# Kernel tuning notes

Hardware: AMD Instinct MI355X
Metric: run time of the kernel (lower is better)

## Reference

```python
import jax, jax.numpy as jnp
import numpy as np

B, LIMG, LTXT = 1, 2048, 256
H, NH, HD = 3072, 24, 128
MLP = int(H * 4.0)
EPS = 1e-6


def setup_inputs() -> dict:
    key = jax.random.key(0)
    ks = iter(jax.random.split(key, 64))
    rn = lambda shape, s=0.02: jax.random.normal(next(ks), shape, jnp.float32) * s
    inp = {
        'img': jax.random.normal(next(ks), (B, LIMG, H), jnp.float32),
        'txt': jax.random.normal(next(ks), (B, LTXT, H), jnp.float32),
        'vec': jax.random.normal(next(ks), (B, H), jnp.float32),
        'pe': jax.random.normal(next(ks), (1, 1, LTXT + LIMG, HD // 2, 2, 2), jnp.float32),
    }
    for p in ('img', 'txt'):
        inp[f'{p}_mod_w'] = rn((H, 6 * H)); inp[f'{p}_mod_b'] = jnp.zeros((6 * H,), jnp.float32)
        inp[f'{p}_ln1_s'] = jnp.ones((H,), jnp.float32); inp[f'{p}_ln1_b'] = jnp.zeros((H,), jnp.float32)
        inp[f'{p}_qkv_w'] = rn((H, 3 * H)); inp[f'{p}_qkv_b'] = jnp.zeros((3 * H,), jnp.float32)
        inp[f'{p}_qn'] = jnp.ones((HD,), jnp.float32); inp[f'{p}_kn'] = jnp.ones((HD,), jnp.float32)
        inp[f'{p}_proj_w'] = rn((H, H)); inp[f'{p}_proj_b'] = jnp.zeros((H,), jnp.float32)
        inp[f'{p}_ln2_s'] = jnp.ones((H,), jnp.float32); inp[f'{p}_ln2_b'] = jnp.zeros((H,), jnp.float32)
        inp[f'{p}_mlp_w1'] = rn((H, MLP)); inp[f'{p}_mlp_b1'] = jnp.zeros((MLP,), jnp.float32)
        inp[f'{p}_mlp_w2'] = rn((MLP, H)); inp[f'{p}_mlp_b2'] = jnp.zeros((H,), jnp.float32)
    return inp


def _ln(x, s, b):
    m = jnp.mean(x, -1, keepdims=True)
    v = jnp.mean((x - m) ** 2, -1, keepdims=True)
    return (x - m) * jax.lax.rsqrt(v + EPS) * s + b


def _rms(x, s):
    return x * jax.lax.rsqrt(jnp.mean(x * x, -1, keepdims=True) + EPS) * s


def _apply_rope(x, pe):
    # x: (B,NH,L,HD); pe: (1,1,L,HD/2,2,2)
    xr = x.reshape(*x.shape[:-1], HD // 2, 1, 2)
    out = pe[..., 0] * xr[..., 0] + pe[..., 1] * xr[..., 1]  # (B,NH,L,HD/2,2)
    return out.reshape(x.shape)


def _attention(q, k, v, pe):
    q = _apply_rope(q, pe)
    k = _apply_rope(k, pe)
    scores = jnp.einsum('bhqd,bhkd->bhqk', q, k) / jnp.sqrt(jnp.float32(HD))
    a = jax.nn.softmax(scores, axis=-1)
    x = jnp.einsum('bhqk,bhkd->bhqd', a, v)  # (B,NH,L,HD)
    return x.transpose(0, 2, 1, 3).reshape(x.shape[0], x.shape[2], NH * HD)


def _mod(vec, w, b):
    o = jnp.dot(jax.nn.silu(vec), w) + b          # (B, 6H)
    return jnp.split(o[:, None, :], 6, axis=-1)


def _qkv_heads(x, w, b, qn, kn):
    Bx, L, _ = x.shape
    qkv = (jnp.dot(x, w) + b).reshape(Bx, L, 3, NH, HD).transpose(2, 0, 3, 1, 4)
    q, k, v = qkv[0], qkv[1], qkv[2]
    return _rms(q, qn), _rms(k, kn), v


def reference(img, txt, vec, pe,
              img_mod_w, img_mod_b, img_ln1_s, img_ln1_b, img_qkv_w, img_qkv_b,
              img_qn, img_kn, img_proj_w, img_proj_b, img_ln2_s, img_ln2_b,
              img_mlp_w1, img_mlp_b1, img_mlp_w2, img_mlp_b2,
              txt_mod_w, txt_mod_b, txt_ln1_s, txt_ln1_b, txt_qkv_w, txt_qkv_b,
              txt_qn, txt_kn, txt_proj_w, txt_proj_b, txt_ln2_s, txt_ln2_b,
              txt_mlp_w1, txt_mlp_b1, txt_mlp_w2, txt_mlp_b2):
    i_sh1, i_sc1, i_g1, i_sh2, i_sc2, i_g2 = _mod(vec, img_mod_w, img_mod_b)
    t_sh1, t_sc1, t_g1, t_sh2, t_sc2, t_g2 = _mod(vec, txt_mod_w, txt_mod_b)

    img_mod = (1 + i_sc1) * _ln(img, img_ln1_s, img_ln1_b) + i_sh1
    txt_mod = (1 + t_sc1) * _ln(txt, txt_ln1_s, txt_ln1_b) + t_sh1

    iq, ik, iv = _qkv_heads(img_mod, img_qkv_w, img_qkv_b, img_qn, img_kn)
    tq, tk, tv = _qkv_heads(txt_mod, txt_qkv_w, txt_qkv_b, txt_qn, txt_kn)

    q = jnp.concatenate([tq, iq], axis=2)
    k = jnp.concatenate([tk, ik], axis=2)
    v = jnp.concatenate([tv, iv], axis=2)
    attn = _attention(q, k, v, pe)  # (B, Ltxt+Limg, H)
    Lt = txt.shape[1]
    txt_attn, img_attn = attn[:, :Lt], attn[:, Lt:]

    img = img + i_g1 * (jnp.dot(img_attn, img_proj_w) + img_proj_b)
    h = (1 + i_sc2) * _ln(img, img_ln2_s, img_ln2_b) + i_sh2
    img = img + i_g2 * (jnp.dot(jax.nn.gelu(jnp.dot(h, img_mlp_w1) + img_mlp_b1), img_mlp_w2) + img_mlp_b2)

    txt = txt + t_g1 * (jnp.dot(txt_attn, txt_proj_w) + txt_proj_b)
    h = (1 + t_sc2) * _ln(txt, txt_ln2_s, txt_ln2_b) + t_sh2
    txt = txt + t_g2 * (jnp.dot(jax.nn.gelu(jnp.dot(h, txt_mlp_w1) + txt_mlp_b1), txt_mlp_w2) + txt_mlp_b2)
    return (img, txt)
```

## Files before the change

### kernel.cpp

```cpp
#include <hip/hip_runtime.h>
#include <hip/hip_bf16.h>
#include <cstdint>

typedef __attribute__((ext_vector_type(8))) short s16x8;
typedef __attribute__((ext_vector_type(4))) short s16x4;
typedef __attribute__((ext_vector_type(2))) short s16x2;
typedef __attribute__((ext_vector_type(4))) float f32x4;

#define LTXT 256
#define LIMG 2048
#define LTOT 2304
#define HDIM 3072
#define NHEADS 24
#define HD 128
#define MLPD 12288

__device__ __forceinline__ short f2bf(float f) {
  union { float f; uint32_t u; } v; v.f = f;
  uint32_t r = v.u + 0x7FFFu + ((v.u >> 16) & 1u);
  return (short)(r >> 16);
}
__device__ __forceinline__ float bf2f(short s) {
  union { uint32_t u; float f; } v; v.u = ((uint32_t)(uint16_t)s) << 16;
  return v.f;
}

#define GLDS16(gsrc, ldst)                                                   \
  __builtin_amdgcn_global_load_lds(                                          \
      (const __attribute__((address_space(1))) uint32_t*)(gsrc),             \
      (__attribute__((address_space(3))) uint32_t*)(ldst), 16, 0, 0)

__global__ __launch_bounds__(256)
void wconv(const float* __restrict__ Wf, short* __restrict__ Wt, int K, int N)
{
  __shared__ short Ls[64][68];
  const int t = threadIdx.x;
  const int k0 = blockIdx.x * 64, n0 = blockIdx.y * 64;
  #pragma unroll
  for (int rep = 0; rep < 4; ++rep) {
    int idx = rep * 256 + t;
    int k = idx >> 4;
    int n = (idx & 15) * 4;
    float4 v = *(const float4*)(Wf + (size_t)(k0 + k) * N + n0 + n);
    Ls[k][n + 0] = f2bf(v.x); Ls[k][n + 1] = f2bf(v.y);
    Ls[k][n + 2] = f2bf(v.z); Ls[k][n + 3] = f2bf(v.w);
  }
  __syncthreads();
  #pragma unroll
  for (int rep = 0; rep < 4; ++rep) {
    int idx = rep * 256 + t;
    int n = idx >> 4;
    int k = (idx & 15) * 4;
    s16x4 o = { Ls[k + 0][n], Ls[k + 1][n], Ls[k + 2][n], Ls[k + 3][n] };
    *(s16x4*)(Wt + (size_t)(n0 + n) * K + k0 + k) = o;
  }
}

__global__ __launch_bounds__(256)
void mod_gemv(const float* __restrict__ vec,
              const float* __restrict__ w_img, const float* __restrict__ b_img,
              const float* __restrict__ w_txt, const float* __restrict__ b_txt,
              float* __restrict__ mod_img, float* __restrict__ mod_txt)
{
  __shared__ float sv[HDIM];
  const int t = threadIdx.x;
  for (int i = t; i < HDIM; i += 256) {
    float x = vec[i];
    sv[i] = x / (1.f + __expf(-x));
  }
  __syncthreads();
  const float* w = blockIdx.y ? w_txt : w_img;
  const float* bb = blockIdx.y ? b_txt : b_img;
  float* o = blockIdx.y ? mod_txt : mod_img;
  const int lane = t & 63, kc = t >> 6;
  const int colbase = blockIdx.x * 256 + lane * 4;
  f32x4 acc = {0.f, 0.f, 0.f, 0.f};
  const float* wp = w + (size_t)kc * 768 * 18432 + colbase;
  #pragma unroll 4
  for (int k = 0; k < 768; ++k) {
    float4 wv = *(const float4*)wp;
    float s = sv[kc * 768 + k];
    acc[0] += s * wv.x; acc[1] += s * wv.y;
    acc[2] += s * wv.z; acc[3] += s * wv.w;
    wp += 18432;
  }
  __shared__ f32x4 part[4][64];
  part[kc][lane] = acc;
  __syncthreads();
  if (t < 64) {
    f32x4 r = part[0][t];
    #pragma unroll
    for (int c = 1; c < 4; ++c) r += part[c][t];
    int cb = blockIdx.x * 256 + t * 4;
    float4 bv = *(const float4*)(bb + cb);
    float4 ov; ov.x = r[0] + bv.x; ov.y = r[1] + bv.y;
    ov.z = r[2] + bv.z; ov.w = r[3] + bv.w;
    *(float4*)(o + cb) = ov;
  }
}

__global__ __launch_bounds__(256)
void ln_mod(const float* __restrict__ xi, const float* __restrict__ xt, int rows_img,
            const float* __restrict__ si, const float* __restrict__ bi,
            const float* __restrict__ st, const float* __restrict__ bt,
            const float* __restrict__ modi, const float* __restrict__ modt,
            int sh_chunk, int sc_chunk,
            short* __restrict__ oi, short* __restrict__ ot)
{
  const int row = blockIdx.x;
  const float *x, *s, *b, *mod;
  short* out;
  if (row < rows_img) {
    x = xi + (size_t)row * HDIM; s = si; b = bi; mod = modi;
    out = oi + (size_t)row * HDIM;
  } else {
    int lr = row - rows_img;
    x = xt + (size_t)lr * HDIM; s = st; b = bt; mod = modt;
    out = ot + (size_t)lr * HDIM;
  }
  const float* sh = mod + (size_t)sh_chunk * HDIM;
  const float* sc = mod + (size_t)sc_chunk * HDIM;
  const int t = threadIdx.x;
  float xv[12];
  {
    float4 a = *(const float4*)(x + t * 12 + 0);
    float4 c = *(const float4*)(x + t * 12 + 4);
    float4 d = *(const float4*)(x + t * 12 + 8);
    xv[0]=a.x; xv[1]=a.y; xv[2]=a.z; xv[3]=a.w;
    xv[4]=c.x; xv[5]=c.y; xv[6]=c.z; xv[7]=c.w;
    xv[8]=d.x; xv[9]=d.y; xv[10]=d.z; xv[11]=d.w;
  }
  float sum = 0.f, ss = 0.f;
  #pragma unroll
  for (int e = 0; e < 12; ++e) { sum += xv[e]; ss += xv[e] * xv[e]; }
  for (int xm = 1; xm < 64; xm <<= 1) {
    sum += __shfl_xor(sum, xm);
    ss  += __shfl_xor(ss, xm);
  }
  __shared__ float red[8];
  const int w = t >> 6, lane = t & 63;
  if (lane == 0) { red[w] = sum; red[4 + w] = ss; }
  __syncthreads();
  sum = red[0] + red[1] + red[2] + red[3];
  ss  = red[4] + red[5] + red[6] + red[7];
  const float mean = sum * (1.f / HDIM);
  const float var = ss * (1.f / HDIM) - mean * mean;
  const float rs = rsqrtf(var + 1e-6f);
  short ov[12];
  #pragma unroll
  for (int e = 0; e < 12; ++e) {
    int c = t * 12 + e;
    float y = (xv[e] - mean) * rs * s[c] + b[c];
    ov[e] = f2bf((1.f + sc[c]) * y + sh[c]);
  }
  #pragma unroll
  for (int j = 0; j < 3; ++j) {
    s16x4 v = { ov[j*4+0], ov[j*4+1], ov[j*4+2], ov[j*4+3] };
    *(s16x4*)(out + t * 12 + j * 4) = v;
  }
}

template<int EPI>
__global__ __launch_bounds__(512, 2)
void gemm256(const short* __restrict__ A, int K, int N, int split,
             const short* __restrict__ W0, const short* __restrict__ W1,
             const float* __restrict__ b0, const float* __restrict__ b1,
             void* __restrict__ out0, void* __restrict__ out1,
             const float* __restrict__ r0, const float* __restrict__ r1,
             const float* __restrict__ g0, const float* __restrict__ g1)
{
  __shared__ __align__(16) short lds[2 * 32768];
  const int tid = threadIdx.x;
  const int lane = tid & 63, w = tid >> 6;
  const int wm = w >> 2, wn = w & 3;
  const int l15 = lane & 15, lg = lane >> 4;
  const int x7 = lane & 7;
  const int bm = blockIdx.x;
  const bool is1 = bm >= split;
  const int m0 = bm * 256, n0 = blockIdx.y * 256;
  const short* WT = is1 ? W1 : W0;
  const float* bias = is1 ? b1 : b0;
  const int nt = K >> 6;

  const int srow = w * 8 + (lane >> 3);
  const int lcw = (lane & 7) ^ (lane >> 3);

  f32x4 acc[8][4];
  #pragma unroll
  for (int i = 0; i < 8; ++i)
    #pragma unroll
    for (int j = 0; j < 4; ++j)
      acc[i][j] = f32x4{0.f, 0.f, 0.f, 0.f};

  auto stage = [&](int tt, int cb) {
    short* LA = &lds[cb * 32768];
    short* LB = LA + 16384;
    const size_t kk = (size_t)tt * 64;
    #pragma unroll
    for (int cc = 0; cc < 4; ++cc) {
      const int rr = cc * 64 + srow;
      GLDS16(A + (size_t)(m0 + rr) * K + kk + lcw * 8, LA + (cc * 512 + w * 64) * 8);
      GLDS16(WT + (size_t)(n0 + rr) * K + kk + lcw * 8, LB + (cc * 512 + w * 64) * 8);
    }
  };

  stage(0, 0);
  stage(1, 1);

  const int rA0 = wm * 128 + l15;
  const int rB0 = wn * 64 + l15;

  for (int t = 0; t < nt; ++t) {
    const int c = t & 1;
    if (t == nt - 1) { asm volatile("s_waitcnt vmcnt(0)" ::: "memory"); }
    else             { asm volatile("s_waitcnt vmcnt(8)" ::: "memory"); }
    __builtin_amdgcn_s_barrier();
    __builtin_amdgcn_sched_barrier(0);
    const short* As = &lds[c * 32768];
    const short* Bs = As + 16384;
    #pragma unroll
    for (int ks = 0; ks < 2; ++ks) {
      const int cofs = ((ks * 4 + lg) ^ x7) * 8;
      s16x8 av[8], bv[4];
      #pragma unroll
      for (int mf = 0; mf < 8; ++mf)
        av[mf] = *(const s16x8*)(As + (rA0 + mf * 16) * 64 + cofs);
      #pragma unroll
      for (int nf = 0; nf < 4; ++nf)
        bv[nf] = *(const s16x8*)(Bs + (rB0 + nf * 16) * 64 + cofs);
      __builtin_amdgcn_s_setprio(1);
      #pragma unroll
      for (int mf = 0; mf < 8; ++mf)
        #pragma unroll
        for (int nf = 0; nf < 4; ++nf)
          acc[mf][nf] = __builtin_amdgcn_mfma_f32_16x16x32_bf16(
              av[mf], bv[nf], acc[mf][nf], 0, 0, 0);
      __builtin_amdgcn_s_setprio(0);
    }
    asm volatile("s_waitcnt lgkmcnt(0)" ::: "memory");
    __builtin_amdgcn_s_barrier();
    __builtin_amdgcn_sched_barrier(0);
    if (t + 2 < nt) stage(t + 2, c);
  }

  const int lrbase = m0 - (is1 ? split * 256 : 0);
  #pragma unroll
  for (int mf = 0; mf < 8; ++mf)
    #pragma unroll
    for (int nf = 0; nf < 4; ++nf) {
      int col = n0 + wn * 64 + nf * 16 + l15;
      float bvs = bias[col];
      #pragma unroll
      for (int r = 0; r < 4; ++r) {
        int row = lrbase + wm * 128 + mf * 16 + lg * 4 + r;
        float x = acc[mf][nf][r] + bvs;
        if constexpr (EPI == 0) {
          short* o = (short*)(is1 ? out1 : out0);
          o[(size_t)row * N + col] = f2bf(x);
        } else if constexpr (EPI == 1) {
          float g = 0.5f * x * (1.f + tanhf(0.7978845608028654f * (x + 0.044715f * x * x * x)));
          short* o = (short*)(is1 ? out1 : out0);
          o[(size_t)row * N + col] = f2bf(g);
        } else if constexpr (EPI == 2) {
          const float* resid = is1 ? r1 : r0;
          const float* gate = is1 ? g1 : g0;
          float* o = (float*)(is1 ? out1 : out0);
          o[(size_t)row * N + col] = resid[(size_t)row * N + col] + gate[col] * x;
        } else {
          const float* gate = is1 ? g1 : g0;
          float* o = (float*)(is1 ? out1 : out0);
          size_t ix = (size_t)row * N + col;
          o[ix] = o[ix] + gate[col] * x;
        }
      }
    }
}

__global__ __launch_bounds__(256)
void qkvr(const short* __restrict__ qkv, const float* __restrict__ pe,
          const float* __restrict__ qn_img, const float* __restrict__ kn_img,
          const float* __restrict__ qn_txt, const float* __restrict__ kn_txt,
          short* __restrict__ Qh, short* __restrict__ Kh)
{
  const int w = threadIdx.x >> 6, lane = threadIdx.x & 63;
  const int tok = blockIdx.x * 4 + w;
  const int h = blockIdx.y;
  const float* qn = (tok < LTXT) ? qn_txt : qn_img;
  const float* kn = (tok < LTXT) ? kn_txt : kn_img;
  const size_t base = (size_t)tok * 9216 + (size_t)h * HD + lane * 2;
  const float4 p4 = *(const float4*)(pe + ((size_t)tok * 64 + lane) * 4);
  {
    s16x2 qs = *(const s16x2*)(qkv + base);
    float x0 = bf2f(qs[0]), x1 = bf2f(qs[1]);
    float sq = x0 * x0 + x1 * x1;
    for (int xm = 1; xm < 64; xm <<= 1) sq += __shfl_xor(sq, xm);
    float r = rsqrtf(sq * (1.f / HD) + 1e-6f);
    x0 = x0 * r * qn[lane * 2]; x1 = x1 * r * qn[lane * 2 + 1];
    s16x2 o = { f2bf(p4.x * x0 + p4.y * x1), f2bf(p4.z * x0 + p4.w * x1) };
    *(s16x2*)(Qh + ((size_t)h * LTOT + tok) * HD + lane * 2) = o;
  }
  {
    s16x2 ks = *(const s16x2*)(qkv + base + HDIM);
    float x0 = bf2f(ks[0]), x1 = bf2f(ks[1]);
    float sq = x0 * x0 + x1 * x1;
    for (int xm = 1; xm < 64; xm <<= 1) sq += __shfl_xor(sq, xm);
    float r = rsqrtf(sq * (1.f / HD) + 1e-6f);
    x0 = x0 * r * kn[lane * 2]; x1 = x1 * r * kn[lane * 2 + 1];
    s16x2 o = { f2bf(p4.x * x0 + p4.y * x1), f2bf(p4.z * x0 + p4.w * x1) };
    *(s16x2*)(Kh + ((size_t)h * LTOT + tok) * HD + lane * 2) = o;
  }
}

__global__ __launch_bounds__(256)
void vt_k(const short* __restrict__ qkv, short* __restrict__ VT)
{
  __shared__ __align__(16) short Vs[64][136];
  const int h = blockIdx.y, tok0 = blockIdx.x * 64;
  const int t = threadIdx.x;
  #pragma unroll
  for (int rep = 0; rep < 4; ++rep) {
    int idx = rep * 256 + t;
    int tk = idx >> 4, oct = idx & 15;
    *(s16x8*)(&Vs[tk][oct * 8]) =
        *(const s16x8*)(qkv + (size_t)(tok0 + tk) * 9216 + 6144 + (size_t)h * HD + oct * 8);
  }
  __syncthreads();
  #pragma unroll
  for (int rep = 0; rep < 4; ++rep) {
    int idx = rep * 256 + t;
    int d = idx >> 3, tg = idx & 7;
    s16x8 o;
    #pragma unroll
    for (int j = 0; j < 8; ++j) o[j] = Vs[tg * 8 + j][d];
    *(s16x8*)(VT + ((size_t)h * HD + d) * LTOT + tok0 + tg * 8) = o;
  }
}

__global__ __launch_bounds__(256, 2)
void attn_k(const short* __restrict__ Qh, const short* __restrict__ Kh,
            const short* __restrict__ VT, short* __restrict__ out)
{
  __shared__ __align__(16) short Ps[4][32][72];
  const int t = threadIdx.x, lane = t & 63, w = t >> 6;
  const int l15 = lane & 15, lg = lane >> 4;
  const int h = blockIdx.y;
  const int qrow = blockIdx.x * 128 + w * 32;

  s16x8 qf[2][4];
  #pragma unroll
  for (int mf = 0; mf < 2; ++mf)
    #pragma unroll
    for (int ks = 0; ks < 4; ++ks)
      qf[mf][ks] = *(const s16x8*)(Qh + ((size_t)h * LTOT + qrow + mf * 16 + l15) * HD + ks * 32 + lg * 8);

  f32x4 O[2][8];
  #pragma unroll
  for (int mf = 0; mf < 2; ++mf)
    #pragma unroll
    for (int dt = 0; dt < 8; ++dt) O[mf][dt] = f32x4{0.f, 0.f, 0.f, 0.f};
  float mrow[2][4], lrow[2][4];
  #pragma unroll
  for (int mf = 0; mf < 2; ++mf)
    #pragma unroll
    for (int r = 0; r < 4; ++r) { mrow[mf][r] = -1e30f; lrow[mf][r] = 0.f; }

  for (int kt = 0; kt < LTOT / 64; ++kt) {
    const int k0 = kt * 64;
    f32x4 S[2][4];
    #pragma unroll
    for (int mf = 0; mf < 2; ++mf)
      #pragma unroll
      for (int jt = 0; jt < 4; ++jt) S[mf][jt] = f32x4{0.f, 0.f, 0.f, 0.f};
    #pragma unroll
    for (int ks = 0; ks < 4; ++ks)
      #pragma unroll
      for (int jt = 0; jt < 4; ++jt) {
        s16x8 kf = *(const s16x8*)(Kh + ((size_t)h * LTOT + k0 + jt * 16 + l15) * HD + ks * 32 + lg * 8);
        S[0][jt] = __builtin_amdgcn_mfma_f32_16x16x32_bf16(qf[0][ks], kf, S[0][jt], 0, 0, 0);
        S[1][jt] = __builtin_amdgcn_mfma_f32_16x16x32_bf16(qf[1][ks], kf, S[1][jt], 0, 0, 0);
      }
    #pragma unroll
    for (int mf = 0; mf < 2; ++mf) {
      const float scl = 0.08838834764831845f;
      #pragma unroll
      for (int jt = 0; jt < 4; ++jt) S[mf][jt] *= scl;
      float pm[4];
      #pragma unroll
      for (int r = 0; r < 4; ++r)
        pm[r] = fmaxf(fmaxf(S[mf][0][r], S[mf][1][r]), fmaxf(S[mf][2][r], S[mf][3][r]));
      for (int xm = 1; xm < 16; xm <<= 1)
        #pragma unroll
        for (int r = 0; r < 4; ++r) pm[r] = fmaxf(pm[r], __shfl_xor(pm[r], xm));
      f32x4 corrv;
      #pragma unroll
      for (int r = 0; r < 4; ++r) {
        float mn = fmaxf(mrow[mf][r], pm[r]);
        corrv[r] = __expf(mrow[mf][r] - mn);
        mrow[mf][r] = mn;
      }
      float rs[4] = {0.f, 0.f, 0.f, 0.f};
      #pragma unroll
      for (int jt = 0; jt < 4; ++jt)
        #pragma unroll
        for (int r = 0; r < 4; ++r) {
          float p = __expf(S[mf][jt][r] - mrow[mf][r]);
          S[mf][jt][r] = p;
          rs[r] += p;
        }
      for (int xm = 1; xm < 16; xm <<= 1)
        #pragma unroll
        for (int r = 0; r < 4; ++r) rs[r] += __shfl_xor(rs[r], xm);
      #pragma unroll
      for (int r = 0; r < 4; ++r) lrow[mf][r] = lrow[mf][r] * corrv[r] + rs[r];
      #pragma unroll
      for (int dt = 0; dt < 8; ++dt) O[mf][dt] *= corrv;
      #pragma unroll
      for (int jt = 0; jt < 4; ++jt)
        #pragma unroll
        for (int r = 0; r < 4; ++r)
          Ps[w][mf * 16 + lg * 4 + r][jt * 16 + l15] = f2bf(S[mf][jt][r]);
    }
    asm volatile("s_waitcnt lgkmcnt(0)" ::: "memory");
    __builtin_amdgcn_sched_barrier(0);
    #pragma unroll
    for (int kk2 = 0; kk2 < 2; ++kk2) {
      s16x8 pf0 = *(const s16x8*)(&Ps[w][l15][kk2 * 32 + lg * 8]);
      s16x8 pf1 = *(const s16x8*)(&Ps[w][16 + l15][kk2 * 32 + lg * 8]);
      #pragma unroll
      for (int dt = 0; dt < 8; ++dt) {
        s16x8 vf = *(const s16x8*)(VT + ((size_t)h * HD + dt * 16 + l15) * LTOT + k0 + kk2 * 32 + lg * 8);
        O[0][dt] = __builtin_amdgcn_mfma_f32_16x16x32_bf16(pf0, vf, O[0][dt], 0, 0, 0);
        O[1][dt] = __builtin_amdgcn_mfma_f32_16x16x32_bf16(pf1, vf, O[1][dt], 0, 0, 0);
      }
    }
    asm volatile("s_waitcnt lgkmcnt(0)" ::: "memory");
    __builtin_amdgcn_sched_barrier(0);
  }
  #pragma unroll
  for (int mf = 0; mf < 2; ++mf) {
    f32x4 inv;
    #pragma unroll
    for (int r = 0; r < 4; ++r) inv[r] = 1.f / lrow[mf][r];
    #pragma unroll
    for (int dt = 0; dt < 8; ++dt) {
      f32x4 o = O[mf][dt] * inv;
      #pragma unroll
      for (int r = 0; r < 4; ++r)
        out[(size_t)(qrow + mf * 16 + lg * 4 + r) * HDIM + (size_t)h * HD + dt * 16 + l15] = f2bf(o[r]);
    }
  }
}

extern "C" void kernel_launch(void* const* d_in, const int* in_sizes, int n_in,
                              void* d_out, int out_size, void* d_ws, size_t ws_size,
                              hipStream_t stream)
{
  (void)in_sizes; (void)n_in; (void)out_size;
  const float* img = (const float*)d_in[0];
  const float* txt = (const float*)d_in[1];
  const float* vec = (const float*)d_in[2];
  const float* pe  = (const float*)d_in[3];
  const float* Pi[16]; const float* Pt[16];
  for (int i = 0; i < 16; ++i) Pi[i] = (const float*)d_in[4 + i];
  for (int i = 0; i < 16; ++i) Pt[i] = (const float*)d_in[20 + i];

  char* ws = (char*)d_ws;
  float* MODI = (float*)(ws + 0);
  float* MODT = (float*)(ws + 73728);
  short* XMI  = (short*)(ws + 147456);
  short* XMT  = (short*)(ws + 12730368);
  short* QKV  = (short*)(ws + 14303232);
  short* QHh  = (short*)(ws + 56770560);
  short* KHh  = (short*)(ws + 70926336);
  short* VTt  = (short*)(ws + 85082112);
  short* ATT  = (short*)(ws + 99237888);
  short* H1   = (short*)(ws + 14303232);
  short* WTA  = (short*)(ws + 113393664);
  short* WTB  = (short*)(ws + 188891136);
  if (ws_size < (size_t)264388608) return;
  float* outI = (float*)d_out;
  float* outT = outI + (size_t)LIMG * HDIM;

  mod_gemv<<<dim3(72, 2), 256, 0, stream>>>(vec, Pi[0], Pi[1], Pt[0], Pt[1], MODI, MODT);
  ln_mod<<<dim3(LTOT), 256, 0, stream>>>(img, txt, LIMG, Pi[2], Pi[3], Pt[2], Pt[3],
                                         MODI, MODT, 0, 1, XMI, XMT);
  wconv<<<dim3(48, 144), 256, 0, stream>>>(Pi[4], WTA, HDIM, 3 * HDIM);
  wconv<<<dim3(48, 144), 256, 0, stream>>>(Pt[4], WTB, HDIM, 3 * HDIM);
  gemm256<0><<<dim3(9, 36), 512, 0, stream>>>(XMI, HDIM, 3 * HDIM, 8,
      WTA, WTB, Pi[5], Pt[5],
      QKV + (size_t)LTXT * 9216, QKV, nullptr, nullptr, nullptr, nullptr);
  qkvr<<<dim3(LTOT / 4, NHEADS), 256, 0, stream>>>(QKV, pe, Pi[6], Pi[7], Pt[6], Pt[7], QHh, KHh);
  vt_k<<<dim3(LTOT / 64, NHEADS), 256, 0, stream>>>(QKV, VTt);
  attn_k<<<dim3(LTOT / 128, NHEADS), 256, 0, stream>>>(QHh, KHh, VTt, ATT);
  wconv<<<dim3(48, 48), 256, 0, stream>>>(Pt[8], WTA, HDIM, HDIM);
  wconv<<<dim3(48, 48), 256, 0, stream>>>(Pi[8], WTB, HDIM, HDIM);
  gemm256<2><<<dim3(9, 12), 512, 0, stream>>>(ATT, HDIM, HDIM, 1,
      WTA, WTB, Pt[9], Pi[9], outT, outI, txt, img,
      MODT + 2 * HDIM, MODI + 2 * HDIM);
  ln_mod<<<dim3(LTOT), 256, 0, stream>>>(outI, outT, LIMG, Pi[10], Pi[11], Pt[10], Pt[11],
                                         MODI, MODT, 3, 4, XMI, XMT);
  wconv<<<dim3(48, 192), 256, 0, stream>>>(Pi[12], WTA, HDIM, MLPD);
  wconv<<<dim3(48, 192), 256, 0, stream>>>(Pt[12], WTB, HDIM, MLPD);
  gemm256<1><<<dim3(9, 48), 512, 0, stream>>>(XMI, HDIM, MLPD, 8,
      WTA, WTB, Pi[13], Pt[13],
      H1, H1 + (size_t)LIMG * MLPD, nullptr, nullptr, nullptr, nullptr);
  wconv<<<dim3(192, 48), 256, 0, stream>>>(Pi[14], WTA, MLPD, HDIM);
  wconv<<<dim3(192, 48), 256, 0, stream>>>(Pt[14], WTB, MLPD, HDIM);
  gemm256<3><<<dim3(9, 12), 512, 0, stream>>>(H1, MLPD, HDIM, 8,
      WTA, WTB, Pi[15], Pt[15], outI, outT, nullptr, nullptr,
      MODI + 5 * HDIM, MODT + 5 * HDIM);
}
```

Baseline: 1.672 ms.

## Restructure GEMM mainloop into interleaved half-K stages with XCD-aware block remap

Splits each 64-wide K tile into two 32-wide halves with a new LDS layout and swizzle. The mainloop becomes four barrier-separated phases that interleave LDS fragment loads, global-to-LDS prefetch of the next halves, and MFMA quads. This is meant to overlap memory traffic with compute more finely and to reduce register pressure, since only four A fragments are held at a time. It also remaps workgroup IDs so neighbouring tiles land on the same XCD for better L2 reuse. In exchange it adds many more barriers and relies on fragile vmcnt bookkeeping.

New measurement: 1.545 ms. -7.6%, faster.

```diff
diff --git a/kernel.cpp b/kernel.cpp
--- a/kernel.cpp
+++ b/kernel.cpp
@@ -169,22 +169,26 @@
              const float* __restrict__ r0, const float* __restrict__ r1,
              const float* __restrict__ g0, const float* __restrict__ g1)
 {
-  __shared__ __align__(16) short lds[2 * 32768];
+  __shared__ __align__(16) short lds[65536];
   const int tid = threadIdx.x;
   const int lane = tid & 63, w = tid >> 6;
   const int wm = w >> 2, wn = w & 3;
   const int l15 = lane & 15, lg = lane >> 4;
-  const int x7 = lane & 7;
-  const int bm = blockIdx.x;
+
+  const int gx = gridDim.x;
+  const int nwg = gx * gridDim.y;
+  const int lin = blockIdx.y * gx + blockIdx.x;
+  const int q8 = nwg >> 3, r8 = nwg & 7;
+  const int xcd = lin & 7, loc = lin >> 3;
+  const int nid = (xcd < r8 ? xcd * (q8 + 1) : r8 * (q8 + 1) + (xcd - r8) * q8) + loc;
+  const int bm = nid % gx, bn = nid / gx;
+
   const bool is1 = bm >= split;
-  const int m0 = bm * 256, n0 = blockIdx.y * 256;
+  const int m0 = bm * 256, n0 = bn * 256;
   const short* WT = is1 ? W1 : W0;
   const float* bias = is1 ? b1 : b0;
   const int nt = K >> 6;
 
-  const int srow = w * 8 + (lane >> 3);
-  const int lcw = (lane & 7) ^ (lane >> 3);
-
   f32x4 acc[8][4];
   #pragma unroll
   for (int i = 0; i < 8; ++i)
@@ -192,55 +196,100 @@
     for (int j = 0; j < 4; ++j)
       acc[i][j] = f32x4{0.f, 0.f, 0.f, 0.f};
 
-  auto stage = [&](int tt, int cb) {
-    short* LA = &lds[cb * 32768];
-    short* LB = LA + 16384;
-    const size_t kk = (size_t)tt * 64;
-    #pragma unroll
-    for (int cc = 0; cc < 4; ++cc) {
-      const int rr = cc * 64 + srow;
-      GLDS16(A + (size_t)(m0 + rr) * K + kk + lcw * 8, LA + (cc * 512 + w * 64) * 8);
-      GLDS16(WT + (size_t)(n0 + rr) * K + kk + lcw * 8, LB + (cc * 512 + w * 64) * 8);
+  auto stage_item = [&](const short* mat, int grow0, int tt, int kh, int ldsOff) {
+    const int kb = tt * 64 + kh * 32;
+    #pragma unroll
+    for (int l = 0; l < 2; ++l) {
+      const int chrow = w * 32 + l * 16 + (lane >> 2);
+      const int lc = (lane & 3) ^ ((chrow >> 1) & 3);
+      GLDS16(mat + (size_t)(grow0 + chrow) * K + kb + lc * 8,
+             lds + ldsOff + (w * 2 + l) * 512);
     }
   };
-
-  stage(0, 0);
-  stage(1, 1);
 
   const int rA0 = wm * 128 + l15;
   const int rB0 = wn * 64 + l15;
+  const int cofs = (lg ^ ((l15 >> 1) & 3)) * 8;
+
+  s16x8 av[4], bv[4];
+  auto ldA4 = [&](int c, int ks, int mfb) {
+    const short* base = lds + c * 32768 + ks * 8192;
+    #pragma unroll
+    for (int i = 0; i < 4; ++i)
+      av[i] = *(const s16x8*)(base + (rA0 + (mfb + i) * 16) * 32 + cofs);
+  };
+  auto ldB4 = [&](int c, int ks) {
+    const short* base = lds + c * 32768 + 16384 + ks * 8192;
+    #pragma unroll
+    for (int i = 0; i < 4; ++i)
+      bv[i] = *(const s16x8*)(base + (rB0 + i * 16) * 32 + cofs);
+  };
+  auto quad = [&](int mfb) {
+    __builtin_amdgcn_s_setprio(1);
+    #pragma unroll
+    for (int i = 0; i < 4; ++i)
+      #pragma unroll
+      for (int j = 0; j < 4; ++j)
+        acc[mfb + i][j] = __builtin_amdgcn_mfma_f32_16x16x32_bf16(
+            av[i], bv[j], acc[mfb + i][j], 0, 0, 0);
+    __builtin_amdgcn_s_setprio(0);
+  };
+
+  stage_item(A, m0, 0, 0, 0);
+  stage_item(WT, n0, 0, 0, 16384);
+  stage_item(A, m0, 0, 1, 8192);
+  stage_item(WT, n0, 0, 1, 24576);
+  if (nt > 1) {
+    stage_item(A, m0, 1, 0, 32768);
+    stage_item(WT, n0, 1, 0, 49152);
+  }
+  asm volatile("s_waitcnt vmcnt(8)" ::: "memory");
+  __builtin_amdgcn_s_barrier();
+  __builtin_amdgcn_sched_barrier(0);
 
   for (int t = 0; t < nt; ++t) {
     const int c = t & 1;
-    if (t == nt - 1) { asm volatile("s_waitcnt vmcnt(0)" ::: "memory"); }
-    else             { asm volatile("s_waitcnt vmcnt(8)" ::: "memory"); }
-    __builtin_amdgcn_s_barrier();
-    __builtin_amdgcn_sched_barrier(0);
-    const short* As = &lds[c * 32768];
-    const short* Bs = As + 16384;
-    #pragma unroll
-    for (int ks = 0; ks < 2; ++ks) {
-      const int cofs = ((ks * 4 + lg) ^ x7) * 8;
-      s16x8 av[8], bv[4];
-      #pragma unroll
-      for (int mf = 0; mf < 8; ++mf)
-        av[mf] = *(const s16x8*)(As + (rA0 + mf * 16) * 64 + cofs);
-      #pragma unroll
-      for (int nf = 0; nf < 4; ++nf)
-        bv[nf] = *(const s16x8*)(Bs + (rB0 + nf * 16) * 64 + cofs);
-      __builtin_amdgcn_s_setprio(1);
-      #pragma unroll
-      for (int mf = 0; mf < 8; ++mf)
-        #pragma unroll
-        for (int nf = 0; nf < 4; ++nf)
-          acc[mf][nf] = __builtin_amdgcn_mfma_f32_16x16x32_bf16(
-              av[mf], bv[nf], acc[mf][nf], 0, 0, 0);
-      __builtin_amdgcn_s_setprio(0);
-    }
-    asm volatile("s_waitcnt lgkmcnt(0)" ::: "memory");
-    __builtin_amdgcn_s_barrier();
-    __builtin_amdgcn_sched_barrier(0);
-    if (t + 2 < nt) stage(t + 2, c);
+    const int cb = c * 32768, cnb = (c ^ 1) * 32768;
+    ldA4(c, 0, 0);
+    ldB4(c, 0);
+    if (t + 1 < nt) stage_item(A, m0, t + 1, 1, cnb + 8192);
+    __builtin_amdgcn_s_barrier();
+    __builtin_amdgcn_sched_barrier(0);
+    quad(0);
+    __builtin_amdgcn_s_barrier();
+    __builtin_amdgcn_sched_barrier(0);
+    ldA4(c, 0, 4);
+    if (t + 1 < nt) {
+      stage_item(WT, n0, t + 1, 1, cnb + 24576);
+      asm volatile("s_waitcnt vmcnt(8)" ::: "memory");
+    } else {
+      asm volatile("s_waitcnt vmcnt(0)" ::: "memory");
+    }
+    __builtin_amdgcn_s_barrier();
+    __builtin_amdgcn_sched_barrier(0);
+    quad(4);
+    __builtin_amdgcn_s_barrier();
+    __builtin_amdgcn_sched_barrier(0);
+    ldA4(c, 1, 0);
+    ldB4(c, 1);
+    if (t + 2 < nt) stage_item(A, m0, t + 2, 0, cb);
+    __builtin_amdgcn_s_barrier();
+    __builtin_amdgcn_sched_barrier(0);
+    quad(0);
+    __builtin_amdgcn_s_barrier();
+    __builtin_amdgcn_sched_barrier(0);
+    ldA4(c, 1, 4);
+    if (t + 2 < nt) {
+      stage_item(WT, n0, t + 2, 0, cb + 16384);
+      asm volatile("s_waitcnt vmcnt(8)" ::: "memory");
+    } else if (t + 1 < nt) {
+      asm volatile("s_waitcnt vmcnt(4)" ::: "memory");
+    }
+    __builtin_amdgcn_s_barrier();
+    __builtin_amdgcn_sched_barrier(0);
+    quad(4);
+    __builtin_amdgcn_s_barrier();
+    __builtin_amdgcn_sched_barrier(0);
   }
 
   const int lrbase = m0 - (is1 ? split * 256 : 0);
```
